# Optimization experiments

Hardware: AMD Instinct MI355X
Metric: run time of the kernel (lower is better)

The kernel has to match this reference:

```python
import jax, jax.numpy as jnp
import numpy as np

B, C, N = 4, 256, 4096
QK = 32  # query/key channel dim hardcoded in module


def setup_inputs() -> dict:
    key = jax.random.key(0)
    ks = jax.random.split(key, 5)
    sc = 1.0 / np.sqrt(C)
    return {
        "x": jax.random.normal(ks[0], (B, C, N), dtype=jnp.float32),
        "Wf": jax.random.normal(ks[1], (QK, C), dtype=jnp.float32) * sc,
        "bf": jnp.zeros((QK,), dtype=jnp.float32),
        "Wg": jax.random.normal(ks[2], (QK, C), dtype=jnp.float32) * sc,
        "bg": jnp.zeros((QK,), dtype=jnp.float32),
        "Wh": jax.random.normal(ks[3], (C, C), dtype=jnp.float32) * sc,
        "bh": jnp.zeros((C,), dtype=jnp.float32),
        "gamma": jax.random.normal(ks[4], (1,), dtype=jnp.float32) * 0.1,
    }


def reference(x, Wf, bf, Wg, bg, Wh, bh, gamma):
    # 1x1 Conv1d == channel-mixing matmul: (O,C) x (B,C,N) -> (B,O,N)
    f = jnp.einsum('oc,bcn->bon', Wf, x) + bf[:, None]   # (B, 32, N)
    g = jnp.einsum('oc,bcn->bon', Wg, x) + bg[:, None]   # (B, 32, N)
    h = jnp.einsum('oc,bcn->bon', Wh, x) + bh[:, None]   # (B, C, N)
    # attention[b, n, m] = sum_k f[b,k,n] * g[b,k,m]  (unscaled, per source)
    attn = jax.nn.softmax(jnp.einsum('bkn,bkm->bnm', f, g), axis=-1)  # (B,N,N)
    # torch.bmm(h, attention): out[b,c,m] = sum_n h[b,c,n] * attn[b,n,m]
    sa = jnp.einsum('bcn,bnm->bcm', h, attn)             # (B, C, N)
    return gamma * sa + x
```

## Files before the change

### kernel.cpp

```cpp
#include <hip/hip_runtime.h>
#include <hip/hip_bf16.h>
#include <math.h>

constexpr int Bb = 4;
constexpr int Cc = 256;
constexpr int Nn = 4096;
constexpr int K  = 32;

constexpr float LOG2E = 1.4426950408889634f;
constexpr float C40L  = 40.0f * LOG2E;

typedef __attribute__((ext_vector_type(8))) short short8;
typedef __attribute__((ext_vector_type(4))) float f32x4;
typedef __attribute__((ext_vector_type(2))) unsigned int uint2v;

static __device__ __forceinline__ unsigned int pack2(float a, float b) {
  union { __hip_bfloat162 h2; unsigned int u; } cv;
  cv.h2 = __float22bfloat162_rn(float2{a, b});
  return cv.u;
}
static __device__ __forceinline__ unsigned short f2bf(float f) {
  union { __hip_bfloat16 h; unsigned short u; } cv;
  cv.h = __float2bfloat16(f);
  return cv.u;
}
static __device__ __forceinline__ f32x4 MF(short8 a, short8 b, f32x4 c) {
  return __builtin_amdgcn_mfma_f32_16x16x32_bf16(a, b, c, 0, 0, 0);
}
static __device__ __forceinline__ float ex2(float v) {
  return __builtin_amdgcn_exp2f(v);
}


__global__ __launch_bounds__(256) void castW(
    const float* __restrict__ Wh, unsigned short* __restrict__ Whb)
{
  int i = (blockIdx.x * 256 + threadIdx.x) * 4;
  float4 v = *(const float4*)&Wh[i];
  uint2 o = { pack2(v.x, v.y), pack2(v.z, v.w) };
  *(uint2*)&Whb[i] = o;
}

__global__ __launch_bounds__(256) void castFG(
    const float* __restrict__ Wf, const float* __restrict__ Wg,
    unsigned short* __restrict__ Wfgb)
{
  int g = (blockIdx.x * 256 + threadIdx.x) * 4;
  int row = g >> 8, c = g & 255;
  const float* src = (row < 32) ? &Wf[row*Cc + c] : &Wg[(row-32)*Cc + c];
  float4 v = *(const float4*)src;
  uint2 o = { pack2(v.x, v.y), pack2(v.z, v.w) };
  *(uint2*)&Wfgb[g] = o;
}

__global__ __launch_bounds__(256) void trans_k(
    const float* __restrict__ x, unsigned short* __restrict__ xT)
{
  __shared__ unsigned short Ls[64][65];
  const int b  = blockIdx.z;
  const int n0 = blockIdx.x * 64, c0 = blockIdx.y * 64;
  const int tid = threadIdx.x;
  {
    const int cr = tid >> 4, n4 = (tid & 15) * 4;
#pragma unroll
    for (int rr = 0; rr < 4; ++rr) {
      int c = rr * 16 + cr;
      float4 v = *(const float4*)&x[(size_t)(b*Cc + c0 + c)*Nn + n0 + n4];
      Ls[c][n4+0] = f2bf(v.x); Ls[c][n4+1] = f2bf(v.y);
      Ls[c][n4+2] = f2bf(v.z); Ls[c][n4+3] = f2bf(v.w);
    }
  }
  __syncthreads();
  {
    const int nw = tid >> 4, cw = (tid & 15) * 4;
#pragma unroll
    for (int rr = 0; rr < 4; ++rr) {
      int n = nw + rr * 16;
      unsigned int lo = (unsigned int)Ls[cw+0][n] | ((unsigned int)Ls[cw+1][n] << 16);
      unsigned int hi = (unsigned int)Ls[cw+2][n] | ((unsigned int)Ls[cw+3][n] << 16);
      uint2 o = { lo, hi };
      *(uint2*)&xT[(size_t)(b*Nn + n0 + n)*Cc + c0 + cw] = o;
    }
  }
}

__global__ __launch_bounds__(256) void proj_fgM(
    const unsigned short* __restrict__ xT, const unsigned short* __restrict__ Wfgb,
    const float* __restrict__ bf, const float* __restrict__ bg,
    unsigned short* __restrict__ Ft, unsigned short* __restrict__ Gt)
{
  const int b = blockIdx.y;
  const int tid = threadIdx.x, wave = tid >> 6, lane = tid & 63;
  const int q = lane >> 4, col = lane & 15;
  const int n = blockIdx.x * 64 + wave * 16 + col;

  const unsigned short* Bp = xT + (size_t)(b*Nn + n)*Cc + q*8;
  const f32x4 zero = {0.f,0.f,0.f,0.f};
  f32x4 af0 = zero, af1 = zero, ag0 = zero, ag1 = zero;
#pragma unroll
  for (int kc = 0; kc < 8; ++kc) {
    short8 bn = *(const short8*)(Bp + kc*32);
    short8 a0 = *(const short8*)(Wfgb + (size_t)( 0 + col)*Cc + kc*32 + q*8);
    short8 a1 = *(const short8*)(Wfgb + (size_t)(16 + col)*Cc + kc*32 + q*8);
    short8 a2 = *(const short8*)(Wfgb + (size_t)(32 + col)*Cc + kc*32 + q*8);
    short8 a3 = *(const short8*)(Wfgb + (size_t)(48 + col)*Cc + kc*32 + q*8);
    af0 = MF(a0, bn, af0); af1 = MF(a1, bn, af1);
    ag0 = MF(a2, bn, ag0); ag1 = MF(a3, bn, ag1);
  }
  float4 bf0 = *(const float4*)&bf[q*4],      bf1 = *(const float4*)&bf[16 + q*4];
  float4 bg0 = *(const float4*)&bg[q*4],      bg1 = *(const float4*)&bg[16 + q*4];
  uint2 F0 = { pack2((af0[0]+bf0.x)*LOG2E, (af0[1]+bf0.y)*LOG2E),
               pack2((af0[2]+bf0.z)*LOG2E, (af0[3]+bf0.w)*LOG2E) };
  uint2 F1 = { pack2((af1[0]+bf1.x)*LOG2E, (af1[1]+bf1.y)*LOG2E),
               pack2((af1[2]+bf1.z)*LOG2E, (af1[3]+bf1.w)*LOG2E) };
  uint2 G0 = { pack2(ag0[0]+bg0.x, ag0[1]+bg0.y), pack2(ag0[2]+bg0.z, ag0[3]+bg0.w) };
  uint2 G1 = { pack2(ag1[0]+bg1.x, ag1[1]+bg1.y), pack2(ag1[2]+bg1.z, ag1[3]+bg1.w) };
  unsigned short* fo = Ft + (size_t)(b*Nn + n)*K;
  unsigned short* go = Gt + (size_t)(b*Nn + n)*K;
  *(uint2*)(fo + q*4) = F0;  *(uint2*)(fo + 16 + q*4) = F1;
  *(uint2*)(go + q*4) = G0;  *(uint2*)(go + 16 + q*4) = G1;
}

__global__ __launch_bounds__(512) void pass1(
    const unsigned short* __restrict__ Ft, const unsigned short* __restrict__ Gt,
    unsigned short* __restrict__ Et, float* __restrict__ Lp)
{
  __shared__ float red[8][64];
  const int n0 = blockIdx.x * 64;
  const int mh = blockIdx.y;
  const int b  = blockIdx.z;
  const int tid = threadIdx.x, wave = tid >> 6, lane = tid & 63;
  const int q = lane >> 4, col = lane & 15;
  const unsigned short* Fb = Ft + (size_t)b*Nn*K;
  const unsigned short* Gb = Gt + (size_t)b*Nn*K;
  unsigned short* Ebt = Et + (size_t)b*Nn*Nn;

  short8 af[4];
#pragma unroll
  for (int rb = 0; rb < 4; ++rb)
    af[rb] = *(const short8*)(Fb + (size_t)(n0 + rb*16 + col)*K + q*8);

  const int mw = mh*2048 + wave*256;
  const f32x4 cinit = {-C40L, -C40L, -C40L, -C40L};
  float l[16];
#pragma unroll
  for (int i = 0; i < 16; ++i) l[i] = 0.f;

  unsigned short* sbase = Ebt + (size_t)(n0 >> 3)*128
                        + (q >> 1)*128 + col*8 + (q & 1)*4;

  short8 gA = *(const short8*)(Gb + (size_t)(mw + col)*K + q*8);
  for (int it = 0; it < 16; ++it) {
    short8 gB = *(const short8*)(Gb + (size_t)(mw + ((it+1)&15)*16 + col)*K + q*8);
    f32x4 ts[4];
    ts[0] = MF(af[0], gA, cinit);
    ts[1] = MF(af[1], gA, cinit);
    ts[2] = MF(af[2], gA, cinit);
    ts[3] = MF(af[3], gA, cinit);
    const int mt = (mw >> 4) + it;
    unsigned short* sb = sbase + (size_t)mt * (Nn*16);
#pragma unroll
    for (int rb = 0; rb < 4; ++rb) {
      float e0 = ex2(ts[rb][0]), e1 = ex2(ts[rb][1]);
      float e2 = ex2(ts[rb][2]), e3 = ex2(ts[rb][3]);
      l[rb*4+0] += e0; l[rb*4+1] += e1; l[rb*4+2] += e2; l[rb*4+3] += e3;
      uint2v w = { pack2(e0, e1), pack2(e2, e3) };
      __builtin_nontemporal_store(w, (uint2v*)(sb + rb*256));
    }
    gA = gB;
  }
#pragma unroll
  for (int d = 1; d < 16; d <<= 1) {
#pragma unroll
    for (int i = 0; i < 16; ++i) l[i] += __shfl_xor(l[i], d);
  }
  if (col == 0) {
#pragma unroll
    for (int rb = 0; rb < 4; ++rb) {
      float4 v = {l[rb*4+0], l[rb*4+1], l[rb*4+2], l[rb*4+3]};
      *(float4*)&red[wave][rb*16 + q*4] = v;
    }
  }
  __syncthreads();
  if (tid < 64) {
    float t = 0.f;
#pragma unroll
    for (int w = 0; w < 8; ++w) t += red[w][tid];
    Lp[((size_t)mh*Bb + b)*Nn + n0 + tid] = t;
  }
}

__global__ __launch_bounds__(256) void sumL(
    const float* __restrict__ Lp, float* __restrict__ L)
{
  int i = blockIdx.x * 256 + threadIdx.x;
  L[i] = Lp[i] + Lp[(size_t)Bb*Nn + i];
}

__global__ __launch_bounds__(256) void proj_hT(
    const unsigned short* __restrict__ xT, const unsigned short* __restrict__ Whb,
    const float* __restrict__ bh, const float* __restrict__ L,
    unsigned short* __restrict__ Ht)
{
  const int b   = blockIdx.z;
  const int n0  = blockIdx.x * 64;
  const int c0  = blockIdx.y * 64;
  const int tid = threadIdx.x;
  const int wave = tid >> 6, lane = tid & 63;
  const int q = lane >> 4, col = lane & 15;
  const int nw = n0 + wave * 16;

  const unsigned short* Arow  = xT  + (size_t)(b*Nn + nw + col) * Cc + q*8;
  const unsigned short* Bbase = Whb + (size_t)(c0 + col) * Cc + q*8;

  const f32x4 zero = {0.f,0.f,0.f,0.f};
  f32x4 acc[4] = {zero, zero, zero, zero};

  short8 a0 = *(const short8*)(Arow);
  short8 b0[4], b1[4];
#pragma unroll
  for (int j = 0; j < 4; ++j) b0[j] = *(const short8*)(Bbase + (size_t)(j*16)*Cc);

  for (int ks = 0; ks < 256; ks += 64) {
    int k1 = (ks + 32) & 255;
    short8 a1 = *(const short8*)(Arow + k1);
#pragma unroll
    for (int j = 0; j < 4; ++j) b1[j] = *(const short8*)(Bbase + (size_t)(j*16)*Cc + k1);
#pragma unroll
    for (int j = 0; j < 4; ++j) acc[j] = MF(a0, b0[j], acc[j]);
    int k2 = (ks + 64) & 255;
    a0 = *(const short8*)(Arow + k2);
#pragma unroll
    for (int j = 0; j < 4; ++j) b0[j] = *(const short8*)(Bbase + (size_t)(j*16)*Cc + k2);
#pragma unroll
    for (int j = 0; j < 4; ++j) acc[j] = MF(a1, b1[j], acc[j]);
  }

  float4 lv = *(const float4*)&L[(size_t)b*Nn + nw + q*4];
  float linv[4] = {1.f/lv.x, 1.f/lv.y, 1.f/lv.z, 1.f/lv.w};
  unsigned short* Hbt = Ht + (size_t)b*Cc*Nn;
  unsigned short* wb = Hbt + (size_t)(nw >> 3)*128 + (q >> 1)*128 + col*8 + (q & 1)*4;
#pragma unroll
  for (int j = 0; j < 4; ++j) {
    float bb = bh[c0 + j*16 + col];
    float v0 = (acc[j][0] + bb) * linv[0];
    float v1 = (acc[j][1] + bb) * linv[1];
    float v2 = (acc[j][2] + bb) * linv[2];
    float v3 = (acc[j][3] + bb) * linv[3];
    uint2v w = { pack2(v0, v1), pack2(v2, v3) };
    *(uint2v*)(wb + (size_t)((c0 >> 4) + j) * (Nn*16)) = w;
  }
}

struct PF { short8 a[8]; short8 e[4]; };

__global__ __launch_bounds__(256, 2) void out_gemm(
    const unsigned short* __restrict__ Ht, const unsigned short* __restrict__ Et,
    const float* __restrict__ x, const float* __restrict__ gamma,
    float* __restrict__ out)
{
  const int id  = blockIdx.x;
  const int xcd = id & 7;
  const int b   = xcd >> 1;
  const int m0  = ((id >> 3) + (xcd & 1) * 64) * 32;
  const int tid = threadIdx.x, wave = tid >> 6, lane = tid & 63;
  const int q = lane >> 4, col = lane & 15;
  const int cg = wave;

  const unsigned short* Hbt = Ht + (size_t)b*Cc*Nn;
  const unsigned short* Ebt = Et + (size_t)b*Nn*Nn;
  const unsigned short* aPtr = Hbt + (size_t)(cg*4)*(Nn*16) + q*128 + col*8;
  const unsigned short* ePtr = Ebt + (size_t)(m0 >> 4)*(Nn*16) + q*128 + col*8;

  const f32x4 zero = {0.f,0.f,0.f,0.f};
  f32x4 acc[4][2];
#pragma unroll
  for (int i = 0; i < 4; ++i) { acc[i][0] = zero; acc[i][1] = zero; }

  PF p0, p1, p2;
  auto ld = [&](PF& P, int nt) {
#pragma unroll
    for (int i = 0; i < 4; ++i) {
      P.a[i*2+0] = *(const short8*)(aPtr + (size_t)i*(Nn*16) + (size_t)nt*16);
      P.a[i*2+1] = *(const short8*)(aPtr + (size_t)i*(Nn*16) + (size_t)(nt+32)*16);
    }
#pragma unroll
    for (int h = 0; h < 2; ++h) {
      P.e[h*2+0] = __builtin_nontemporal_load(
          (const short8*)(ePtr + (size_t)h*(Nn*16) + (size_t)nt*16));
      P.e[h*2+1] = __builtin_nontemporal_load(
          (const short8*)(ePtr + (size_t)h*(Nn*16) + (size_t)(nt+32)*16));
    }
  };
  auto work = [&](const PF& P) {
#pragma unroll
    for (int i = 0; i < 4; ++i) {
#pragma unroll
      for (int h = 0; h < 2; ++h) {
        acc[i][h] = MF(P.a[i*2+0], P.e[h*2+0], acc[i][h]);
        acc[i][h] = MF(P.a[i*2+1], P.e[h*2+1], acc[i][h]);
      }
    }
  };

  ld(p0, 0); ld(p1, 64); ld(p2, 128);
  for (int t = 0; t < 63; t += 3) {
    int n3 = (t+3)*64, n4 = (t+4)*64, n5 = (t+5)*64;
    work(p0); if (n3 < Nn) ld(p0, n3);
    work(p1); if (n4 < Nn) ld(p1, n4);
    work(p2); if (n5 < Nn) ld(p2, n5);
  }
  work(p0);

  const float gm = gamma[0];
#pragma unroll
  for (int i = 0; i < 4; ++i) {
#pragma unroll
    for (int h = 0; h < 2; ++h) {
      const int m = m0 + h*16 + col;
#pragma unroll
      for (int r = 0; r < 4; ++r) {
        int c = cg*64 + i*16 + q*4 + r;
        size_t idx = ((size_t)(b*Cc + c))*Nn + m;
        out[idx] = fmaf(gm, acc[i][h][r], x[idx]);
      }
    }
  }
}

__global__ __launch_bounds__(256) void proj_h(
    const unsigned short* __restrict__ xT, const unsigned short* __restrict__ Whb,
    const float* __restrict__ bh, unsigned short* __restrict__ H)
{
  const int b   = blockIdx.z;
  const int n0  = blockIdx.x * 64;
  const int c0  = blockIdx.y * 64;
  const int tid = threadIdx.x;
  const int wave = tid >> 6, lane = tid & 63;
  const int q = lane >> 4, col = lane & 15;
  const int cw = c0 + wave * 16;

  const unsigned short* Arow = Whb + (size_t)(cw + col) * Cc + q*8;
  const unsigned short* Bbase = xT + (size_t)(b*Nn + n0 + col) * Cc + q*8;

  const f32x4 zero = {0.f,0.f,0.f,0.f};
  f32x4 acc[4] = {zero, zero, zero, zero};

  short8 a0 = *(const short8*)(Arow);
  short8 b0[4], b1[4];
#pragma unroll
  for (int j = 0; j < 4; ++j) b0[j] = *(const short8*)(Bbase + (size_t)(j*16)*Cc);

  for (int ks = 0; ks < 256; ks += 64) {
    int k1 = (ks + 32) & 255;
    short8 a1 = *(const short8*)(Arow + k1);
#pragma unroll
    for (int j = 0; j < 4; ++j) b1[j] = *(const short8*)(Bbase + (size_t)(j*16)*Cc + k1);
#pragma unroll
    for (int j = 0; j < 4; ++j) acc[j] = MF(a0, b0[j], acc[j]);
    int k2 = (ks + 64) & 255;
    a0 = *(const short8*)(Arow + k2);
#pragma unroll
    for (int j = 0; j < 4; ++j) b0[j] = *(const short8*)(Bbase + (size_t)(j*16)*Cc + k2);
#pragma unroll
    for (int j = 0; j < 4; ++j) acc[j] = MF(a1, b1[j], acc[j]);
  }

  float4 bb = *(const float4*)&bh[cw + q*4];
  float brs[4] = {bb.x, bb.y, bb.z, bb.w};
#pragma unroll
  for (int j = 0; j < 4; ++j) {
#pragma unroll
    for (int r = 0; r < 4; ++r) {
      int c = cw + q*4 + r;
      int n = n0 + j*16 + col;
      H[(size_t)(b*Cc + c)*Nn + n] = f2bf(acc[j][r] + brs[r]);
    }
  }
}

__global__ __launch_bounds__(256) void stats_k(
    const unsigned short* __restrict__ Ft, const unsigned short* __restrict__ Gt,
    float* __restrict__ Lp)
{
  __shared__ float red[4][32];
  const int b = blockIdx.y >> 1, ms = blockIdx.y & 1;
  const int n0 = blockIdx.x * 32;
  const int tid = threadIdx.x, wave = tid >> 6, lane = tid & 63;
  const int q = lane >> 4, col = lane & 15;
  const unsigned short* Fb = Ft + (size_t)b*Nn*K;
  const unsigned short* Gb = Gt + (size_t)b*Nn*K;

  short8 af0 = *(const short8*)(Fb + (size_t)(n0      + col)*K + q*8);
  short8 af1 = *(const short8*)(Fb + (size_t)(n0 + 16 + col)*K + q*8);
  const int mq = ms*2048 + wave*512;
  const f32x4 zero = {0.f,0.f,0.f,0.f};
  float l[8] = {0.f,0.f,0.f,0.f,0.f,0.f,0.f,0.f};

  short8 gfA = *(const short8*)(Gb + (size_t)(mq + col)*K + q*8);
  for (int it = 0; it < 32; ++it) {
    short8 gfB = *(const short8*)(Gb + (size_t)(mq + ((it+1)&31)*16 + col)*K + q*8);
    f32x4 s0 = MF(af0, gfA, zero);
    f32x4 s1 = MF(af1, gfA, zero);
#pragma unroll
    for (int r = 0; r < 4; ++r) {
      l[r]   += ex2(s0[r] - C40L);
      l[4+r] += ex2(s1[r] - C40L);
    }
    gfA = gfB;
  }
#pragma unroll
  for (int d = 1; d < 16; d <<= 1) {
#pragma unroll
    for (int r = 0; r < 8; ++r) l[r] += __shfl_xor(l[r], d);
  }
  if (col == 0) {
    float4 v0 = {l[0], l[1], l[2], l[3]};
    float4 v1 = {l[4], l[5], l[6], l[7]};
    *(float4*)&red[wave][q*4]      = v0;
    *(float4*)&red[wave][16 + q*4] = v1;
  }
  __syncthreads();
  if (tid < 32) {
    float t = red[0][tid] + red[1][tid] + red[2][tid] + red[3][tid];
    Lp[((size_t)ms*Bb + b)*Nn + n0 + tid] = t;
  }
}

__global__ __launch_bounds__(256) void zcomb(
    const float* __restrict__ Lp, float* __restrict__ Z2)
{
  int i = blockIdx.x * 256 + threadIdx.x;
  Z2[i] = C40L + __log2f(Lp[i] + Lp[(size_t)Bb*Nn + i]);
}

struct Gen { short8 af0, af1; short8 hf[4]; };

__global__ __launch_bounds__(256, 4) void out_k(
    const unsigned short* __restrict__ Ft, const unsigned short* __restrict__ Gt,
    const unsigned short* __restrict__ H, const float* __restrict__ Z2,
    const float* __restrict__ x, const float* __restrict__ gamma,
    float* __restrict__ dst)
{
  __shared__ unsigned short Ps[4][32*40];
  const int b   = blockIdx.y;
  const int m0  = blockIdx.x * 64;
  const int c0b = blockIdx.z * 128;
  const int tid = threadIdx.x, wave = tid >> 6, lane = tid & 63;
  const int q = lane >> 4, col = lane & 15;
  const int mw  = m0 + (wave & 1) * 32;
  const int c0w = c0b + (wave >> 1) * 64;

  const unsigned short* Fb = Ft + (size_t)b*Nn*K;
  const unsigned short* Hb = H  + (size_t)b*Cc*Nn;
  const float*          Zb = Z2 + (size_t)b*Nn;

  short8 gf0 = *(const short8*)(Gt + (size_t)(b*Nn + mw      + col)*K + q*8);
  short8 gf1 = *(const short8*)(Gt + (size_t)(b*Nn + mw + 16 + col)*K + q*8);

  unsigned short* Pw = &Ps[wave][0];
  const f32x4 zero = {0.f,0.f,0.f,0.f};
  f32x4 acc[2][4];
#pragma unroll
  for (int j = 0; j < 2; ++j)
#pragma unroll
    for (int i = 0; i < 4; ++i) acc[j][i] = zero;

  Gen A, B;
  auto loadGen = [&](Gen& G, int nt) {
    G.af0 = *(const short8*)(Fb + (size_t)(nt      + col)*K + q*8);
    G.af1 = *(const short8*)(Fb + (size_t)(nt + 16 + col)*K + q*8);
#pragma unroll
    for (int i = 0; i < 4; ++i)
      G.hf[i] = *(const short8*)(Hb + (size_t)(c0w + i*16 + col)*Nn + nt + q*8);
  };
  auto step = [&](int nt, Gen& CUR, Gen& NXT) {
    loadGen(NXT, (nt + 32) & (Nn - 1));
    float4 z0 = *(const float4*)(Zb + nt + q*4);
    float4 z1 = *(const float4*)(Zb + nt + 16 + q*4);
    f32x4 s00 = MF(CUR.af0, gf0, zero);
    f32x4 s01 = MF(CUR.af0, gf1, zero);
    f32x4 s10 = MF(CUR.af1, gf0, zero);
    f32x4 s11 = MF(CUR.af1, gf1, zero);
    uint2 w00 = { pack2(ex2(s00[0]-z0.x), ex2(s00[1]-z0.y)),
                  pack2(ex2(s00[2]-z0.z), ex2(s00[3]-z0.w)) };
    uint2 w01 = { pack2(ex2(s01[0]-z0.x), ex2(s01[1]-z0.y)),
                  pack2(ex2(s01[2]-z0.z), ex2(s01[3]-z0.w)) };
    uint2 w10 = { pack2(ex2(s10[0]-z1.x), ex2(s10[1]-z1.y)),
                  pack2(ex2(s10[2]-z1.z), ex2(s10[3]-z1.w)) };
    uint2 w11 = { pack2(ex2(s11[0]-z1.x), ex2(s11[1]-z1.y)),
                  pack2(ex2(s11[2]-z1.z), ex2(s11[3]-z1.w)) };
    *(uint2*)&Pw[(     col)*40      + q*4] = w00;
    *(uint2*)&Pw[(16 + col)*40      + q*4] = w01;
    *(uint2*)&Pw[(     col)*40 + 16 + q*4] = w10;
    *(uint2*)&Pw[(16 + col)*40 + 16 + q*4] = w11;
    short8 pf0 = *(const short8*)&Pw[(     col)*40 + q*8];
    short8 pf1 = *(const short8*)&Pw[(16 + col)*40 + q*8];
#pragma unroll
    for (int i = 0; i < 4; ++i) {
      acc[0][i] = MF(CUR.hf[i], pf0, acc[0][i]);
      acc[1][i] = MF(CUR.hf[i], pf1, acc[1][i]);
    }
  };

  loadGen(A, 0);
  for (int t = 0; t < 128; t += 2) {
    step(t*32,      A, B);
    step(t*32 + 32, B, A);
  }

  const float gm = gamma[0];
#pragma unroll
  for (int mj = 0; mj < 2; ++mj) {
    const int m = mw + mj*16 + col;
#pragma unroll
    for (int i = 0; i < 4; ++i) {
#pragma unroll
      for (int r = 0; r < 4; ++r) {
        int c = c0w + i*16 + q*4 + r;
        size_t idx = ((size_t)(b*Cc + c))*Nn + m;
        dst[idx] = fmaf(gm, acc[mj][i][r], x[idx]);
      }
    }
  }
}

extern "C" void kernel_launch(void* const* d_in, const int* in_sizes, int n_in,
                              void* d_out, int out_size, void* d_ws, size_t ws_size,
                              hipStream_t stream) {
  (void)in_sizes; (void)n_in; (void)out_size;
  const float* x     = (const float*)d_in[0];
  const float* Wf    = (const float*)d_in[1];
  const float* bf    = (const float*)d_in[2];
  const float* Wg    = (const float*)d_in[3];
  const float* bg    = (const float*)d_in[4];
  const float* Wh    = (const float*)d_in[5];
  const float* bh    = (const float*)d_in[6];
  const float* gamma = (const float*)d_in[7];
  float* out = (float*)d_out;

  unsigned short* Ft   = (unsigned short*)d_ws;
  unsigned short* Gt   = Ft   + (size_t)Bb*Nn*K;
  unsigned short* xT   = Gt   + (size_t)Bb*Nn*K;
  unsigned short* H    = xT   + (size_t)Bb*Nn*Cc;
  unsigned short* Whb  = H    + (size_t)Bb*Cc*Nn;
  unsigned short* Wfgb = Whb  + (size_t)Cc*Cc;
  float*          L    = (float*)(Wfgb + 64*Cc);
  float*          Z2   = L  + (size_t)Bb*Nn;
  float*          Lp   = Z2 + (size_t)Bb*Nn;
  unsigned short* Et   = (unsigned short*)(Lp + 2*(size_t)Bb*Nn);

  const size_t baseEnd = 19038208ull + 65536ull*4;
  const size_t needE   = baseEnd + (size_t)Bb*Nn*Nn*2;

  castW   <<<dim3(Cc*Cc/1024), 256, 0, stream>>>(Wh, Whb);
  castFG  <<<dim3(64*Cc/1024), 256, 0, stream>>>(Wf, Wg, Wfgb);
  trans_k <<<dim3(Nn/64, Cc/64, Bb), 256, 0, stream>>>(x, xT);
  proj_fgM<<<dim3(Nn/64, Bb), 256, 0, stream>>>(xT, Wfgb, bf, bg, Ft, Gt);

  if (ws_size >= needE) {
    pass1   <<<dim3(Nn/64, 2, Bb), 512, 0, stream>>>(Ft, Gt, Et, Lp);
    sumL    <<<dim3(Bb*Nn/256), 256, 0, stream>>>(Lp, L);
    proj_hT <<<dim3(Nn/64, Cc/64, Bb), 256, 0, stream>>>(xT, Whb, bh, L, H);
    out_gemm<<<dim3(512), 256, 0, stream>>>(H, Et, x, gamma, out);
  } else {
    proj_h  <<<dim3(Nn/64, Cc/64, Bb), 256, 0, stream>>>(xT, Whb, bh, H);
    stats_k <<<dim3(Nn/32, 2*Bb), 256, 0, stream>>>(Ft, Gt, Lp);
    zcomb   <<<dim3(Bb*Nn/256), 256, 0, stream>>>(Lp, Z2);
    out_k   <<<dim3(Nn/64, Bb, 2), 256, 0, stream>>>(Ft, Gt, H, Z2, x, gamma, out);
  }
}
```

Before: 233.9 us.

## Retile output GEMM into 128x128 LDS-staged tiles with direct global-to-LDS loads

```diff
diff --git a/kernel.cpp b/kernel.cpp
--- a/kernel.cpp
+++ b/kernel.cpp
@@ -29,6 +29,12 @@
 }
 static __device__ __forceinline__ float ex2(float v) {
   return __builtin_amdgcn_exp2f(v);
+}
+static __device__ __forceinline__ void stage16(const unsigned short* g,
+                                               unsigned short* l) {
+  __builtin_amdgcn_global_load_lds(
+      (const __attribute__((address_space(1))) unsigned int*)g,
+      (__attribute__((address_space(3))) unsigned int*)l, 16, 0, 0);
 }
 
 
@@ -252,77 +258,93 @@
   }
 }
 
-struct PF { short8 a[8]; short8 e[4]; };
-
-__global__ __launch_bounds__(256, 2) void out_gemm(
+__global__ __launch_bounds__(256) void out_gemm2(
     const unsigned short* __restrict__ Ht, const unsigned short* __restrict__ Et,
     const float* __restrict__ x, const float* __restrict__ gamma,
     float* __restrict__ out)
 {
+  __shared__ unsigned short As[2][8192];
+  __shared__ unsigned short Bs[2][8192];
+  constexpr int TS = Nn * 16;
+
   const int id  = blockIdx.x;
-  const int xcd = id & 7;
-  const int b   = xcd >> 1;
-  const int m0  = ((id >> 3) + (xcd & 1) * 64) * 32;
+  const int xcd = id & 7, s = id >> 3;
+  const int b    = xcd >> 1;
+  const int tile = s + (xcd & 1) * 32;
+  const int c0 = (tile & 1) * 128;
+  const int m0 = (tile >> 1) * 128;
   const int tid = threadIdx.x, wave = tid >> 6, lane = tid & 63;
   const int q = lane >> 4, col = lane & 15;
-  const int cg = wave;
-
-  const unsigned short* Hbt = Ht + (size_t)b*Cc*Nn;
-  const unsigned short* Ebt = Et + (size_t)b*Nn*Nn;
-  const unsigned short* aPtr = Hbt + (size_t)(cg*4)*(Nn*16) + q*128 + col*8;
-  const unsigned short* ePtr = Ebt + (size_t)(m0 >> 4)*(Nn*16) + q*128 + col*8;
+  const int wc = wave & 1, wm = wave >> 1;
+
+  const unsigned short* Ag = Ht + (size_t)b*Cc*Nn + (size_t)(c0 >> 4)*TS;
+  const unsigned short* Bg = Et + (size_t)b*Nn*Nn + (size_t)(m0 >> 4)*TS;
+
+  auto stage = [&](int buf, int k0) {
+    const int kb = (k0 >> 3) * 128;
+    if (wave < 2) {
+      unsigned short* ld = &As[buf][0];
+#pragma unroll
+      for (int i = 0; i < 8; ++i) {
+        int j = wave*8 + i, ct = j >> 1, h2 = j & 1;
+        stage16(Ag + (size_t)ct*TS + kb + h2*512 + lane*8,
+                ld + ct*1024 + h2*512);
+      }
+    } else {
+      unsigned short* ld = &Bs[buf][0];
+#pragma unroll
+      for (int i = 0; i < 8; ++i) {
+        int j = (wave-2)*8 + i, mt = j >> 1, h2 = j & 1;
+        stage16(Bg + (size_t)mt*TS + kb + h2*512 + lane*8,
+                ld + mt*1024 + h2*512);
+      }
+    }
+  };
 
   const f32x4 zero = {0.f,0.f,0.f,0.f};
-  f32x4 acc[4][2];
-#pragma unroll
-  for (int i = 0; i < 4; ++i) { acc[i][0] = zero; acc[i][1] = zero; }
-
-  PF p0, p1, p2;
-  auto ld = [&](PF& P, int nt) {
-#pragma unroll
-    for (int i = 0; i < 4; ++i) {
-      P.a[i*2+0] = *(const short8*)(aPtr + (size_t)i*(Nn*16) + (size_t)nt*16);
-      P.a[i*2+1] = *(const short8*)(aPtr + (size_t)i*(Nn*16) + (size_t)(nt+32)*16);
-    }
-#pragma unroll
-    for (int h = 0; h < 2; ++h) {
-      P.e[h*2+0] = __builtin_nontemporal_load(
-          (const short8*)(ePtr + (size_t)h*(Nn*16) + (size_t)nt*16));
-      P.e[h*2+1] = __builtin_nontemporal_load(
-          (const short8*)(ePtr + (size_t)h*(Nn*16) + (size_t)(nt+32)*16));
+  f32x4 acc[4][4];
+#pragma unroll
+  for (int i = 0; i < 4; ++i)
+#pragma unroll
+    for (int j = 0; j < 4; ++j) acc[i][j] = zero;
+
+  auto compute = [&](int buf) {
+#pragma unroll
+    for (int kc = 0; kc < 2; ++kc) {
+      short8 af[4], ef[4];
+#pragma unroll
+      for (int i = 0; i < 4; ++i) {
+        af[i] = *(const short8*)&As[buf][(wc*4+i)*1024 + (kc*4+q)*128 + col*8];
+        ef[i] = *(const short8*)&Bs[buf][(wm*4+i)*1024 + (kc*4+q)*128 + col*8];
+      }
+#pragma unroll
+      for (int ci = 0; ci < 4; ++ci)
+#pragma unroll
+        for (int mi = 0; mi < 4; ++mi)
+          acc[ci][mi] = MF(af[ci], ef[mi], acc[ci][mi]);
     }
   };
-  auto work = [&](const PF& P) {
-#pragma unroll
-    for (int i = 0; i < 4; ++i) {
-#pragma unroll
-      for (int h = 0; h < 2; ++h) {
-        acc[i][h] = MF(P.a[i*2+0], P.e[h*2+0], acc[i][h]);
-        acc[i][h] = MF(P.a[i*2+1], P.e[h*2+1], acc[i][h]);
-      }
-    }
-  };
-
-  ld(p0, 0); ld(p1, 64); ld(p2, 128);
-  for (int t = 0; t < 63; t += 3) {
-    int n3 = (t+3)*64, n4 = (t+4)*64, n5 = (t+5)*64;
-    work(p0); if (n3 < Nn) ld(p0, n3);
-    work(p1); if (n4 < Nn) ld(p1, n4);
-    work(p2); if (n5 < Nn) ld(p2, n5);
-  }
-  work(p0);
+
+  stage(0, 0);
+  __syncthreads();
+  for (int t = 0; t < 63; ++t) {
+    stage((t + 1) & 1, (t + 1) * 64);
+    compute(t & 1);
+    __syncthreads();
+  }
+  compute(1);
 
   const float gm = gamma[0];
 #pragma unroll
-  for (int i = 0; i < 4; ++i) {
-#pragma unroll
-    for (int h = 0; h < 2; ++h) {
-      const int m = m0 + h*16 + col;
+  for (int ci = 0; ci < 4; ++ci) {
+#pragma unroll
+    for (int mi = 0; mi < 4; ++mi) {
+      const int m = m0 + wm*64 + mi*16 + col;
 #pragma unroll
       for (int r = 0; r < 4; ++r) {
-        int c = cg*64 + i*16 + q*4 + r;
+        int c = c0 + wc*64 + ci*16 + q*4 + r;
         size_t idx = ((size_t)(b*Cc + c))*Nn + m;
-        out[idx] = fmaf(gm, acc[i][h][r], x[idx]);
+        out[idx] = fmaf(gm, acc[ci][mi][r], x[idx]);
       }
     }
   }
@@ -559,10 +581,10 @@
   proj_fgM<<<dim3(Nn/64, Bb), 256, 0, stream>>>(xT, Wfgb, bf, bg, Ft, Gt);
 
   if (ws_size >= needE) {
-    pass1   <<<dim3(Nn/64, 2, Bb), 512, 0, stream>>>(Ft, Gt, Et, Lp);
-    sumL    <<<dim3(Bb*Nn/256), 256, 0, stream>>>(Lp, L);
-    proj_hT <<<dim3(Nn/64, Cc/64, Bb), 256, 0, stream>>>(xT, Whb, bh, L, H);
-    out_gemm<<<dim3(512), 256, 0, stream>>>(H, Et, x, gamma, out);
+    pass1    <<<dim3(Nn/64, 2, Bb), 512, 0, stream>>>(Ft, Gt, Et, Lp);
+    sumL     <<<dim3(Bb*Nn/256), 256, 0, stream>>>(Lp, L);
+    proj_hT  <<<dim3(Nn/64, Cc/64, Bb), 256, 0, stream>>>(xT, Whb, bh, L, H);
+    out_gemm2<<<dim3(256), 256, 0, stream>>>(H, Et, x, gamma, out);
   } else {
     proj_h  <<<dim3(Nn/64, Cc/64, Bb), 256, 0, stream>>>(xT, Whb, bh, H);
     stats_k <<<dim3(Nn/32, 2*Bb), 256, 0, stream>>>(Ft, Gt, Lp);
```

Result: faster. 224.8 us (-3.9%).
